# Performance work log

Measured on AMD Instinct MI355X. Metric: run time of the kernel, lower is better.

Reference implementation:

```python
import jax, jax.numpy as jnp
import numpy as np

N_CLASSES_FG = 20  # n_classes - 1

def _norm(t, axis=1):
    # F.normalize(t, dim=axis, eps=1e-10)
    n = jnp.linalg.norm(t, axis=axis, keepdims=True)
    return t / jnp.maximum(n, 1e-10)

def setup_inputs() -> dict:
    key = jax.random.key(0)
    ks = jax.random.split(key, 6)
    B, C, H, W = 8, 512, 80, 80
    N, Hr, Wr = 100, 40, 40
    return {
        "code_C": jax.random.normal(ks[0], (B, C, H, W), jnp.float32),
        "code_BG": jax.random.normal(ks[1], (B, C, H, W), jnp.float32),
        "ref_code_c": jax.random.normal(ks[2], (N, C, Hr, Wr), jnp.float32),
        "ref_code_bg": jax.random.normal(ks[3], (N, C, Hr, Wr), jnp.float32),
        "sum_patch_coord": jax.random.randint(ks[4], (N, 2), 0, Hr, dtype=jnp.int32),
        "cls_mask": jax.random.randint(ks[5], (N,), 0, N_CLASSES_FG, dtype=jnp.int32),
    }

def reference(code_C, code_BG, ref_code_c, ref_code_bg, sum_patch_coord, cls_mask):
    B, Cdim, H, W = code_C.shape
    N = ref_code_c.shape[0]
    code_C = _norm(code_C)   # channelwise L2 normalize
    code_BG = _norm(code_BG)
    # gather per-annotation feature vectors: ref_code_c[i, :, pc[i,1], pc[i,0]] -> [N, C]
    code_vectors = ref_code_c[jnp.arange(N), :, sum_patch_coord[:, 1], sum_patch_coord[:, 0]]
    # mean-mode prototypes: class-wise mean of gathered vectors
    protos = jax.ops.segment_sum(code_vectors, cls_mask, num_segments=N_CLASSES_FG)  # [V, C]
    counts = jax.ops.segment_sum(jnp.ones((N,), code_vectors.dtype), cls_mask, num_segments=N_CLASSES_FG)
    protos = protos / jnp.maximum(counts, 1.0)[:, None]  # classes with 0 vectors stay zero
    # cosine-similarity maps against normalized prototypes
    prob_C = jnp.einsum('bchw,vc->bvhw', code_C, _norm(protos, axis=1))  # [B, V, H, W]
    # pick the most-background pixel (min of summed class similarity), k=1 topk(-x)
    flat = prob_C.sum(axis=1).reshape(B, -1)  # [B, H*W]
    idx = jnp.argmin(flat, axis=1)
    i_x, i_y = idx // W, idx % W
    min_vec = code_BG[jnp.arange(B), :, i_x, i_y]  # [B, C]
    prob_BG = jnp.einsum('bchw,bc->bhw', code_BG, min_vec)  # [B, H, W]
    probs = jnp.concatenate([prob_BG[:, None], prob_C], axis=1)  # [B, V+1, H, W]
    return jax.nn.softmax(probs, axis=1)
```

## Files before the change

kernel.cpp:

```cpp
#include <hip/hip_runtime.h>
#include <math.h>

#define BB 8
#define CC 512
#define HWSZ 6400
#define NN 100
#define HR 40
#define WR 40
#define VV 20
#define VO 21
#define TPX 256
#define NT (HWSZ / TPX)

typedef unsigned long long u64;
typedef float f4 __attribute__((ext_vector_type(4)));

__device__ __forceinline__ unsigned mapf(float f) {
    unsigned b = __float_as_uint(f);
    return (b & 0x80000000u) ? ~b : (b | 0x80000000u);
}

__global__ __launch_bounds__(512) void k_protos(const float* __restrict__ refc,
                                                const int* __restrict__ coord,
                                                const int* __restrict__ cls,
                                                float* __restrict__ protosT,
                                                u64* __restrict__ batchMin) {
    const int v = blockIdx.x;
    const int c = threadIdx.x;
    if (v == 0 && c < BB) batchMin[c] = ~0ull;

    float acc = 0.f;
    int cnt = 0;
    for (int n = 0; n < NN; ++n) {
        if (cls[n] == v) {
            int y = coord[2 * n + 1];
            int x = coord[2 * n + 0];
            acc += refc[((size_t)(n * CC + c) * HR + y) * WR + x];
            ++cnt;
        }
    }
    acc /= fmaxf((float)cnt, 1.0f);

    float ss = acc * acc;
    #pragma unroll
    for (int off = 32; off; off >>= 1) ss += __shfl_xor(ss, off);
    __shared__ float sW[8];
    const int wave = c >> 6, lane = c & 63;
    if (lane == 0) sW[wave] = ss;
    __syncthreads();
    float tot = 0.f;
    #pragma unroll
    for (int w = 0; w < 8; ++w) tot += sW[w];
    float scale = 1.0f / fmaxf(sqrtf(tot), 1e-10f);

    protosT[c * VV + v] = acc * scale;
}

__global__ __launch_bounds__(256) void k_probC_part(const float* __restrict__ codeC,
                                                    const float* __restrict__ protosT,
                                                    float* __restrict__ partC) {
    __shared__ float red[4 * 11 * TPX];

    const int tid  = threadIdx.x;
    const int w    = tid >> 6, lane = tid & 63;
    const int blk  = blockIdx.x;
    const int cg   = blk & 1;
    const int tile = (blk >> 1) % NT;
    const int b    = blk / (2 * NT);
    const int c0   = __builtin_amdgcn_readfirstlane(cg * 256 + w * 64);

    const float* src = codeC + ((size_t)(b * CC + c0)) * HWSZ + tile * TPX + 4 * lane;
    const float* pt  = protosT + (size_t)c0 * VV;

    f4 d[VV];
    #pragma unroll
    for (int v = 0; v < VV; ++v) d[v] = (f4)(0.f);
    f4 ss = (f4)(0.f);

    #pragma unroll 8
    for (int c = 0; c < 64; ++c) {
        f4 x = __builtin_nontemporal_load((const f4*)(src + (size_t)c * HWSZ));
        ss.x = fmaf(x.x, x.x, ss.x);
        ss.y = fmaf(x.y, x.y, ss.y);
        ss.z = fmaf(x.z, x.z, ss.z);
        ss.w = fmaf(x.w, x.w, ss.w);
        const float* pr = pt + c * VV;
        #pragma unroll
        for (int v = 0; v < VV; ++v) {
            float p = pr[v];
            d[v].x = fmaf(x.x, p, d[v].x);
            d[v].y = fmaf(x.y, p, d[v].y);
            d[v].z = fmaf(x.z, p, d[v].z);
            d[v].w = fmaf(x.w, p, d[v].w);
        }
    }

    float* dstp = partC + (size_t)blk * (VO * TPX);

    *(f4*)&red[(w * 11 + 0) * TPX + 4 * lane] = ss;
    #pragma unroll
    for (int r = 0; r < 10; ++r)
        *(f4*)&red[(w * 11 + 1 + r) * TPX + 4 * lane] = d[r];
    __syncthreads();
    for (int q = tid; q < 11 * TPX; q += 256) {
        float t = red[q] + red[11 * TPX + q] + red[22 * TPX + q] + red[33 * TPX + q];
        dstp[q] = t;
    }
    __syncthreads();

    #pragma unroll
    for (int r = 0; r < 10; ++r)
        *(f4*)&red[(w * 11 + r) * TPX + 4 * lane] = d[10 + r];
    __syncthreads();
    for (int q = tid; q < 10 * TPX; q += 256) {
        float t = red[q] + red[11 * TPX + q] + red[22 * TPX + q] + red[33 * TPX + q];
        dstp[11 * TPX + q] = t;
    }
}

__global__ __launch_bounds__(256) void k_finishC(const float* __restrict__ partC,
                                                 float* __restrict__ probC,
                                                 u64* __restrict__ batchMin) {
    __shared__ u64 sKey[4];
    const int tid  = threadIdx.x;
    const int tile = blockIdx.x % NT;
    const int b    = blockIdx.x / NT;

    const float* p0 = partC + ((size_t)(b * 2 * NT + tile * 2)) * (VO * TPX);
    const float* p1 = p0 + VO * TPX;

    float ssT = p0[tid] + p1[tid];
    float scale = 1.0f / fmaxf(sqrtf(ssT), 1e-10f);

    float psum = 0.f;
    float* dst = probC + (size_t)b * VV * HWSZ + tile * TPX;
    #pragma unroll
    for (int v = 0; v < VV; ++v) {
        float dv = p0[(1 + v) * TPX + tid] + p1[(1 + v) * TPX + tid];
        float pv = dv * scale;
        dst[(size_t)v * HWSZ + tid] = pv;
        psum += pv;
    }

    u64 key = ((u64)mapf(psum) << 32) | (unsigned)(tile * TPX + tid);
    #pragma unroll
    for (int off = 32; off; off >>= 1) {
        u64 o = __shfl_xor(key, off);
        if (o < key) key = o;
    }
    if ((tid & 63) == 0) sKey[tid >> 6] = key;
    __syncthreads();
    if (tid == 0) {
        u64 kk = sKey[0];
        kk = sKey[1] < kk ? sKey[1] : kk;
        kk = sKey[2] < kk ? sKey[2] : kk;
        kk = sKey[3] < kk ? sKey[3] : kk;
        atomicMin(&batchMin[b], kk);
    }
}

__global__ __launch_bounds__(512) void k_minvec(const u64* __restrict__ batchMin,
                                                const float* __restrict__ codeBG,
                                                float* __restrict__ minvecN) {
    const int b = blockIdx.x, c = threadIdx.x;
    const int pix = (int)(unsigned)(batchMin[b] & 0xFFFFFFFFull);
    float x = codeBG[(size_t)(b * CC + c) * HWSZ + pix];
    float ss = x * x;
    #pragma unroll
    for (int off = 32; off; off >>= 1) ss += __shfl_xor(ss, off);
    __shared__ float sW[8];
    if ((c & 63) == 0) sW[c >> 6] = ss;
    __syncthreads();
    float tot = 0.f;
    #pragma unroll
    for (int w = 0; w < 8; ++w) tot += sW[w];
    minvecN[b * CC + c] = x * (1.0f / fmaxf(sqrtf(tot), 1e-10f));
}

__global__ __launch_bounds__(256) void k_bg_part(const float* __restrict__ codeBG,
                                                 const float* __restrict__ minvecN,
                                                 float* __restrict__ partBG) {
    __shared__ float red[4 * 2 * TPX];

    const int tid  = threadIdx.x;
    const int w    = tid >> 6, lane = tid & 63;
    const int blk  = blockIdx.x;
    const int cg   = blk & 1;
    const int tile = (blk >> 1) % NT;
    const int b    = blk / (2 * NT);
    const int c0   = __builtin_amdgcn_readfirstlane(cg * 256 + w * 64);

    const float* src = codeBG + ((size_t)(b * CC + c0)) * HWSZ + tile * TPX + 4 * lane;
    const float* mv  = minvecN + b * CC + c0;

    f4 ss = (f4)(0.f);
    f4 dg = (f4)(0.f);

    #pragma unroll 8
    for (int c = 0; c < 64; ++c) {
        f4 x = __builtin_nontemporal_load((const f4*)(src + (size_t)c * HWSZ));
        float m = mv[c];
        ss.x = fmaf(x.x, x.x, ss.x);
        ss.y = fmaf(x.y, x.y, ss.y);
        ss.z = fmaf(x.z, x.z, ss.z);
        ss.w = fmaf(x.w, x.w, ss.w);
        dg.x = fmaf(x.x, m, dg.x);
        dg.y = fmaf(x.y, m, dg.y);
        dg.z = fmaf(x.z, m, dg.z);
        dg.w = fmaf(x.w, m, dg.w);
    }

    *(f4*)&red[(w * 2 + 0) * TPX + 4 * lane] = ss;
    *(f4*)&red[(w * 2 + 1) * TPX + 4 * lane] = dg;
    __syncthreads();

    float* dstp = partBG + (size_t)blk * (2 * TPX);
    for (int q = tid; q < 2 * TPX; q += 256) {
        float t = red[q] + red[2 * TPX + q] + red[4 * TPX + q] + red[6 * TPX + q];
        dstp[q] = t;
    }
}

__global__ __launch_bounds__(256) void k_finishBG(const float* __restrict__ partBG,
                                                  const float* __restrict__ probC,
                                                  float* __restrict__ out) {
    const int tid  = threadIdx.x;
    const int tile = blockIdx.x % NT;
    const int b    = blockIdx.x / NT;

    const float* q0 = partBG + ((size_t)(b * 2 * NT + tile * 2)) * (2 * TPX);
    const float* q1 = q0 + 2 * TPX;

    float ssT = q0[tid] + q1[tid];
    float dgT = q0[TPX + tid] + q1[TPX + tid];
    float pbg = dgT * (1.0f / fmaxf(sqrtf(ssT), 1e-10f));

    float pv[VO];
    pv[0] = pbg;
    const float* pc = probC + (size_t)b * VV * HWSZ + tile * TPX + tid;
    #pragma unroll
    for (int v = 0; v < VV; ++v) pv[v + 1] = pc[(size_t)v * HWSZ];

    float m = pv[0];
    #pragma unroll
    for (int i = 1; i < VO; ++i) m = fmaxf(m, pv[i]);
    float se = 0.f;
    #pragma unroll
    for (int i = 0; i < VO; ++i) { pv[i] = __expf(pv[i] - m); se += pv[i]; }
    float inv = 1.0f / se;

    float* dstp = out + (size_t)b * VO * HWSZ + tile * TPX + tid;
    #pragma unroll
    for (int i = 0; i < VO; ++i) dstp[(size_t)i * HWSZ] = pv[i] * inv;
}

extern "C" void kernel_launch(void* const* d_in, const int* in_sizes, int n_in,
                              void* d_out, int out_size, void* d_ws, size_t ws_size,
                              hipStream_t stream) {
    const float* codeC  = (const float*)d_in[0];
    const float* codeBG = (const float*)d_in[1];
    const float* refc   = (const float*)d_in[2];
    const int* coord = (const int*)d_in[4];
    const int* cls   = (const int*)d_in[5];
    float* out = (float*)d_out;

    char* ws = (char*)d_ws;
    float* protosT  = (float*)(ws);
    float* probC    = (float*)(ws + 40960);
    float* minvecN  = (float*)(ws + 4136960);
    u64*   batchMin = (u64*)  (ws + 4153344);
    float* partC    = (float*)(ws + 4153408);
    float* partBG   = (float*)(ws + 12755008);

    k_protos    <<<dim3(VV),          dim3(512), 0, stream>>>(refc, coord, cls, protosT, batchMin);
    k_probC_part<<<dim3(BB * NT * 2), dim3(256), 0, stream>>>(codeC, protosT, partC);
    k_finishC   <<<dim3(BB * NT),     dim3(256), 0, stream>>>(partC, probC, batchMin);
    k_minvec    <<<dim3(BB),          dim3(512), 0, stream>>>(batchMin, codeBG, minvecN);
    k_bg_part   <<<dim3(BB * NT * 2), dim3(256), 0, stream>>>(codeBG, minvecN, partBG);
    k_finishBG  <<<dim3(BB * NT),     dim3(256), 0, stream>>>(partBG, probC, out);
}
```

Before: 70.01 us.

## Split channel reduction across 8 blocks and store partial dot products as bf16

Each block now handles one 64-channel group over a 1280-pixel tile and writes its per-group partials straight to global memory, with no in-block LDS reduction. The 20 class partial dots are stored as bf16, alongside fp32 sum-of-squares and the per-pixel class sum. The finish kernels then add up the 8 groups. This is meant to remove the LDS reduction and its barriers and to halve partial-buffer traffic, but it adds bf16 rounding error to the class similarity maps. Non-temporal loads are also replaced with ordinary loads.

```diff
diff --git a/kernel.cpp b/kernel.cpp
--- a/kernel.cpp
+++ b/kernel.cpp
@@ -9,8 +9,11 @@
 #define WR 40
 #define VV 20
 #define VO 21
-#define TPX 256
-#define NT (HWSZ / TPX)
+#define TPX 1280
+#define NTT 5
+#define NG 8
+#define GC 64
+#define THR 320
 
 typedef unsigned long long u64;
 typedef float f4 __attribute__((ext_vector_type(4)));
@@ -18,6 +21,13 @@
 __device__ __forceinline__ unsigned mapf(float f) {
     unsigned b = __float_as_uint(f);
     return (b & 0x80000000u) ? ~b : (b | 0x80000000u);
+}
+__device__ __forceinline__ unsigned short f2bf(float f) {
+    unsigned u = __float_as_uint(f);
+    return (unsigned short)((u + 0x7fffu + ((u >> 16) & 1u)) >> 16);
+}
+__device__ __forceinline__ float bf2f(unsigned short h) {
+    return __uint_as_float(((unsigned)h) << 16);
 }
 
 __global__ __launch_bounds__(512) void k_protos(const float* __restrict__ refc,
@@ -56,21 +66,19 @@
     protosT[c * VV + v] = acc * scale;
 }
 
-__global__ __launch_bounds__(256) void k_probC_part(const float* __restrict__ codeC,
+__global__ __launch_bounds__(THR) void k_probC_part(const float* __restrict__ codeC,
                                                     const float* __restrict__ protosT,
-                                                    float* __restrict__ partC) {
-    __shared__ float red[4 * 11 * TPX];
-
-    const int tid  = threadIdx.x;
-    const int w    = tid >> 6, lane = tid & 63;
+                                                    unsigned short* __restrict__ dBf,
+                                                    float* __restrict__ ssf,
+                                                    float* __restrict__ Sf) {
+    const int t    = threadIdx.x;
     const int blk  = blockIdx.x;
-    const int cg   = blk & 1;
-    const int tile = (blk >> 1) % NT;
-    const int b    = blk / (2 * NT);
-    const int c0   = __builtin_amdgcn_readfirstlane(cg * 256 + w * 64);
-
-    const float* src = codeC + ((size_t)(b * CC + c0)) * HWSZ + tile * TPX + 4 * lane;
-    const float* pt  = protosT + (size_t)c0 * VV;
+    const int g    = blk & 7;
+    const int tile = (blk >> 3) % NTT;
+    const int b    = blk / (NG * NTT);
+
+    const float* src = codeC + ((size_t)(b * CC + g * GC)) * HWSZ + tile * TPX + 4 * t;
+    const float* pt  = protosT + (size_t)(g * GC) * VV;
 
     f4 d[VV];
     #pragma unroll
@@ -78,8 +86,8 @@
     f4 ss = (f4)(0.f);
 
     #pragma unroll 8
-    for (int c = 0; c < 64; ++c) {
-        f4 x = __builtin_nontemporal_load((const f4*)(src + (size_t)c * HWSZ));
+    for (int c = 0; c < GC; ++c) {
+        f4 x = *(const f4*)(src + (size_t)c * HWSZ);
         ss.x = fmaf(x.x, x.x, ss.x);
         ss.y = fmaf(x.y, x.y, ss.y);
         ss.z = fmaf(x.z, x.z, ss.z);
@@ -95,54 +103,53 @@
         }
     }
 
-    float* dstp = partC + (size_t)blk * (VO * TPX);
-
-    *(f4*)&red[(w * 11 + 0) * TPX + 4 * lane] = ss;
-    #pragma unroll
-    for (int r = 0; r < 10; ++r)
-        *(f4*)&red[(w * 11 + 1 + r) * TPX + 4 * lane] = d[r];
-    __syncthreads();
-    for (int q = tid; q < 11 * TPX; q += 256) {
-        float t = red[q] + red[11 * TPX + q] + red[22 * TPX + q] + red[33 * TPX + q];
-        dstp[q] = t;
-    }
-    __syncthreads();
-
-    #pragma unroll
-    for (int r = 0; r < 10; ++r)
-        *(f4*)&red[(w * 11 + r) * TPX + 4 * lane] = d[10 + r];
-    __syncthreads();
-    for (int q = tid; q < 10 * TPX; q += 256) {
-        float t = red[q] + red[11 * TPX + q] + red[22 * TPX + q] + red[33 * TPX + q];
-        dstp[11 * TPX + q] = t;
-    }
-}
-
-__global__ __launch_bounds__(256) void k_finishC(const float* __restrict__ partC,
+    unsigned short* dB = dBf + (size_t)blk * (VV * TPX) + 4 * t;
+    f4 S = (f4)(0.f);
+    #pragma unroll
+    for (int v = 0; v < VV; ++v) {
+        ushort4 h;
+        h.x = f2bf(d[v].x); h.y = f2bf(d[v].y); h.z = f2bf(d[v].z); h.w = f2bf(d[v].w);
+        *(ushort4*)(dB + (size_t)v * TPX) = h;
+        S.x += d[v].x; S.y += d[v].y; S.z += d[v].z; S.w += d[v].w;
+    }
+    *(f4*)(ssf + (size_t)blk * TPX + 4 * t) = ss;
+    *(f4*)(Sf  + (size_t)blk * TPX + 4 * t) = S;
+}
+
+__global__ __launch_bounds__(256) void k_finishC(const unsigned short* __restrict__ dBf,
+                                                 const float* __restrict__ ssf,
+                                                 const float* __restrict__ Sf,
                                                  float* __restrict__ probC,
                                                  u64* __restrict__ batchMin) {
     __shared__ u64 sKey[4];
-    const int tid  = threadIdx.x;
-    const int tile = blockIdx.x % NT;
-    const int b    = blockIdx.x / NT;
-
-    const float* p0 = partC + ((size_t)(b * 2 * NT + tile * 2)) * (VO * TPX);
-    const float* p1 = p0 + VO * TPX;
-
-    float ssT = p0[tid] + p1[tid];
+    const int tid   = threadIdx.x;
+    const int chunk = blockIdx.x % 25;
+    const int b     = blockIdx.x / 25;
+    const int tile  = chunk / 5;
+    const int pxp   = (chunk % 5) * 256 + tid;
+    const int px    = tile * TPX + pxp;
+    const int base  = (b * NTT + tile) * NG;
+
+    float ssT = 0.f, ST = 0.f;
+    #pragma unroll
+    for (int g = 0; g < NG; ++g) {
+        ssT += ssf[(size_t)(base + g) * TPX + pxp];
+        ST  += Sf [(size_t)(base + g) * TPX + pxp];
+    }
     float scale = 1.0f / fmaxf(sqrtf(ssT), 1e-10f);
 
-    float psum = 0.f;
-    float* dst = probC + (size_t)b * VV * HWSZ + tile * TPX;
+    float* dst = probC + (size_t)b * VV * HWSZ + px;
     #pragma unroll
     for (int v = 0; v < VV; ++v) {
-        float dv = p0[(1 + v) * TPX + tid] + p1[(1 + v) * TPX + tid];
-        float pv = dv * scale;
-        dst[(size_t)v * HWSZ + tid] = pv;
-        psum += pv;
-    }
-
-    u64 key = ((u64)mapf(psum) << 32) | (unsigned)(tile * TPX + tid);
+        float dv = 0.f;
+        #pragma unroll
+        for (int g = 0; g < NG; ++g)
+            dv += bf2f(dBf[(size_t)(base + g) * (VV * TPX) + v * TPX + pxp]);
+        dst[(size_t)v * HWSZ] = dv * scale;
+    }
+
+    float psum = ST * scale;
+    u64 key = ((u64)mapf(psum) << 32) | (unsigned)px;
     #pragma unroll
     for (int off = 32; off; off >>= 1) {
         u64 o = __shfl_xor(key, off);
@@ -177,28 +184,24 @@
     minvecN[b * CC + c] = x * (1.0f / fmaxf(sqrtf(tot), 1e-10f));
 }
 
-__global__ __launch_bounds__(256) void k_bg_part(const float* __restrict__ codeBG,
+__global__ __launch_bounds__(THR) void k_bg_part(const float* __restrict__ codeBG,
                                                  const float* __restrict__ minvecN,
-                                                 float* __restrict__ partBG) {
-    __shared__ float red[4 * 2 * TPX];
-
-    const int tid  = threadIdx.x;
-    const int w    = tid >> 6, lane = tid & 63;
+                                                 float* __restrict__ bgf) {
+    const int t    = threadIdx.x;
     const int blk  = blockIdx.x;
-    const int cg   = blk & 1;
-    const int tile = (blk >> 1) % NT;
-    const int b    = blk / (2 * NT);
-    const int c0   = __builtin_amdgcn_readfirstlane(cg * 256 + w * 64);
-
-    const float* src = codeBG + ((size_t)(b * CC + c0)) * HWSZ + tile * TPX + 4 * lane;
-    const float* mv  = minvecN + b * CC + c0;
+    const int g    = blk & 7;
+    const int tile = (blk >> 3) % NTT;
+    const int b    = blk / (NG * NTT);
+
+    const float* src = codeBG + ((size_t)(b * CC + g * GC)) * HWSZ + tile * TPX + 4 * t;
+    const float* mv  = minvecN + b * CC + g * GC;
 
     f4 ss = (f4)(0.f);
     f4 dg = (f4)(0.f);
 
     #pragma unroll 8
-    for (int c = 0; c < 64; ++c) {
-        f4 x = __builtin_nontemporal_load((const f4*)(src + (size_t)c * HWSZ));
+    for (int c = 0; c < GC; ++c) {
+        f4 x = *(const f4*)(src + (size_t)c * HWSZ);
         float m = mv[c];
         ss.x = fmaf(x.x, x.x, ss.x);
         ss.y = fmaf(x.y, x.y, ss.y);
@@ -210,34 +213,32 @@
         dg.w = fmaf(x.w, m, dg.w);
     }
 
-    *(f4*)&red[(w * 2 + 0) * TPX + 4 * lane] = ss;
-    *(f4*)&red[(w * 2 + 1) * TPX + 4 * lane] = dg;
-    __syncthreads();
-
-    float* dstp = partBG + (size_t)blk * (2 * TPX);
-    for (int q = tid; q < 2 * TPX; q += 256) {
-        float t = red[q] + red[2 * TPX + q] + red[4 * TPX + q] + red[6 * TPX + q];
-        dstp[q] = t;
-    }
-}
-
-__global__ __launch_bounds__(256) void k_finishBG(const float* __restrict__ partBG,
+    *(f4*)(bgf + (size_t)blk * (2 * TPX) + 4 * t)       = ss;
+    *(f4*)(bgf + (size_t)blk * (2 * TPX) + TPX + 4 * t) = dg;
+}
+
+__global__ __launch_bounds__(256) void k_finishBG(const float* __restrict__ bgf,
                                                   const float* __restrict__ probC,
                                                   float* __restrict__ out) {
-    const int tid  = threadIdx.x;
-    const int tile = blockIdx.x % NT;
-    const int b    = blockIdx.x / NT;
-
-    const float* q0 = partBG + ((size_t)(b * 2 * NT + tile * 2)) * (2 * TPX);
-    const float* q1 = q0 + 2 * TPX;
-
-    float ssT = q0[tid] + q1[tid];
-    float dgT = q0[TPX + tid] + q1[TPX + tid];
+    const int tid   = threadIdx.x;
+    const int chunk = blockIdx.x % 25;
+    const int b     = blockIdx.x / 25;
+    const int tile  = chunk / 5;
+    const int pxp   = (chunk % 5) * 256 + tid;
+    const int px    = tile * TPX + pxp;
+    const int base  = (b * NTT + tile) * NG;
+
+    float ssT = 0.f, dgT = 0.f;
+    #pragma unroll
+    for (int g = 0; g < NG; ++g) {
+        ssT += bgf[(size_t)(base + g) * (2 * TPX) + pxp];
+        dgT += bgf[(size_t)(base + g) * (2 * TPX) + TPX + pxp];
+    }
     float pbg = dgT * (1.0f / fmaxf(sqrtf(ssT), 1e-10f));
 
     float pv[VO];
     pv[0] = pbg;
-    const float* pc = probC + (size_t)b * VV * HWSZ + tile * TPX + tid;
+    const float* pc = probC + (size_t)b * VV * HWSZ + px;
     #pragma unroll
     for (int v = 0; v < VV; ++v) pv[v + 1] = pc[(size_t)v * HWSZ];
 
@@ -249,7 +250,7 @@
     for (int i = 0; i < VO; ++i) { pv[i] = __expf(pv[i] - m); se += pv[i]; }
     float inv = 1.0f / se;
 
-    float* dstp = out + (size_t)b * VO * HWSZ + tile * TPX + tid;
+    float* dstp = out + (size_t)b * VO * HWSZ + px;
     #pragma unroll
     for (int i = 0; i < VO; ++i) dstp[(size_t)i * HWSZ] = pv[i] * inv;
 }
@@ -265,17 +266,19 @@
     float* out = (float*)d_out;
 
     char* ws = (char*)d_ws;
-    float* protosT  = (float*)(ws);
-    float* probC    = (float*)(ws + 40960);
-    float* minvecN  = (float*)(ws + 4136960);
-    u64*   batchMin = (u64*)  (ws + 4153344);
-    float* partC    = (float*)(ws + 4153408);
-    float* partBG   = (float*)(ws + 12755008);
-
-    k_protos    <<<dim3(VV),          dim3(512), 0, stream>>>(refc, coord, cls, protosT, batchMin);
-    k_probC_part<<<dim3(BB * NT * 2), dim3(256), 0, stream>>>(codeC, protosT, partC);
-    k_finishC   <<<dim3(BB * NT),     dim3(256), 0, stream>>>(partC, probC, batchMin);
-    k_minvec    <<<dim3(BB),          dim3(512), 0, stream>>>(batchMin, codeBG, minvecN);
-    k_bg_part   <<<dim3(BB * NT * 2), dim3(256), 0, stream>>>(codeBG, minvecN, partBG);
-    k_finishBG  <<<dim3(BB * NT),     dim3(256), 0, stream>>>(partBG, probC, out);
-}
+    float*          protosT  = (float*)         (ws);
+    float*          probC    = (float*)         (ws + 40960);
+    float*          minvecN  = (float*)         (ws + 4136960);
+    u64*            batchMin = (u64*)           (ws + 4153344);
+    float*          ssf      = (float*)         (ws + 4153408);
+    float*          Sf       = (float*)         (ws + 5791808);
+    unsigned short* dBf      = (unsigned short*)(ws + 7430208);
+    float*          bgf      = (float*)         (ws + 7430208);
+
+    k_protos    <<<dim3(VV),        dim3(512), 0, stream>>>(refc, coord, cls, protosT, batchMin);
+    k_probC_part<<<dim3(BB*NTT*NG), dim3(THR), 0, stream>>>(codeC, protosT, dBf, ssf, Sf);
+    k_finishC   <<<dim3(BB*25),     dim3(256), 0, stream>>>(dBf, ssf, Sf, probC, batchMin);
+    k_minvec    <<<dim3(BB),        dim3(512), 0, stream>>>(batchMin, codeBG, minvecN);
+    k_bg_part   <<<dim3(BB*NTT*NG), dim3(THR), 0, stream>>>(codeBG, minvecN, bgf);
+    k_finishBG  <<<dim3(BB*25),     dim3(256), 0, stream>>>(bgf, probC, out);
+}
```

After: 101.1 us. +44.5%, slower.
